# Performance work log

Hardware: AMD Instinct MI355X
Metric: run time of the kernel (lower is better)

## Reference

```python
import jax, jax.numpy as jnp
import numpy as np

B, C, H, W = 16, 256, 32, 32
NUM_LAYERS = 30
OUT = 16  # sqrt(out_channels)
EPS = 1e-5


def setup_inputs() -> dict:
    key = jax.random.key(0)
    k1, k2, k3 = jax.random.split(key, 3)
    x = jax.random.normal(k1, (B, C, H, W), dtype=jnp.float32)
    # delta_t ~ small positive values (module inits ~N(0.01, 0.005))
    delta_t = jax.random.uniform(k2, (NUM_LAYERS, 1), dtype=jnp.float32) * 0.02
    matrices = jax.random.normal(k3, (NUM_LAYERS, 1, 1, OUT, OUT), dtype=jnp.float32) * 0.1
    gamma = jnp.ones((H * W,), dtype=jnp.float32)   # BatchNorm2d weight, oc = i*i = H*W
    beta = jnp.zeros((H * W,), dtype=jnp.float32)   # BatchNorm2d bias
    return {"x": x, "delta_t": delta_t, "matrices": matrices, "gamma": gamma, "beta": beta}


def _bn_relu6(z, gamma, beta):
    # training-mode BatchNorm2d over channel axis 1 (channels = H*W), then ReLU6
    mean = jnp.mean(z, axis=(0, 2, 3), keepdims=True)
    var = jnp.mean(jnp.square(z - mean), axis=(0, 2, 3), keepdims=True)  # biased var
    zhat = (z - mean) * jax.lax.rsqrt(var + EPS)
    g = gamma.reshape(1, -1, 1, 1)
    b = beta.reshape(1, -1, 1, 1)
    return jnp.clip(zhat * g + b, 0.0, 6.0)


def reference(x, delta_t, matrices, gamma, beta):
    b, c, h, w = x.shape
    hw = h * w
    # feature_reshape: [B,C,H,W] -> [B,HW,C] -> [B,HW,out,out] (inn == out branch)
    x1 = x.reshape(b, c, hw).transpose(0, 2, 1).reshape(b, hw, OUT, OUT)
    dt = jnp.clip(delta_t, 0.0, 6.0)[:, 0]  # relu6(delta_t), shape [L]

    def step(y0, params):
        m, dtl = params  # m: [1,1,out,out] broadcasts elementwise against x1
        dydt = -y0 + _bn_relu6(y0 + m * x1, gamma, beta)
        return y0 + dtl * dydt, None

    y0, _ = jax.lax.scan(step, x1, (matrices, dt))
    # (y0 + x1): [B, HW, out, out] -> view [B,H,W,out*out] -> permute to [B,out*out,H,W]
    y = (y0 + x1).reshape(b, h, w, OUT * OUT).transpose(0, 3, 1, 2)
    return y
```

## Files before the change

### kernel.cpp

```cpp
#include <hip/hip_runtime.h>

typedef float v2f __attribute__((ext_vector_type(2)));
typedef float v4f __attribute__((ext_vector_type(4)));

#define HW      1024
#define NLAYERS 30
#define TPB     512

template <int CTRL, int RMASK>
__device__ __forceinline__ float dpp_add(float x) {
    int t = __builtin_amdgcn_update_dpp(0, __builtin_bit_cast(int, x),
                                        CTRL, RMASK, 0xf, true);
    return x + __builtin_bit_cast(float, t);
}
__device__ __forceinline__ float wave_sum64(float x) {
    x = dpp_add<0x111, 0xf>(x);
    x = dpp_add<0x112, 0xf>(x);
    x = dpp_add<0x114, 0xf>(x);
    x = dpp_add<0x118, 0xf>(x);
    x = dpp_add<0x142, 0xa>(x);
    x = dpp_add<0x143, 0xc>(x);
    return x;
}

__global__ __launch_bounds__(TPB, 4) void ode2ch(
    const float* __restrict__ x, const float* __restrict__ delta_t,
    const float* __restrict__ matrices, const float* __restrict__ gamma,
    const float* __restrict__ beta, float* __restrict__ out) {

    const int bid = blockIdx.x;
    const int gs  = ((bid & 7) << 6) | (bid >> 3);
    const int p0  = gs << 1;
    const int t   = threadIdx.x;
    const int c   = t & 255;
    const int bb0 = t >> 8;
    const int wid = t >> 6;
    const int lane = t & 63;

    __shared__ v4f red[2][8];

    v2f x1[8], y[8], z[8];
#pragma unroll
    for (int i = 0; i < 8; ++i) {
        const size_t off = (size_t)((2 * i + bb0) * 256 + c) * HW + p0;
        x1[i] = *(const v2f*)(x + off);
        y[i]  = x1[i];
    }

    const v2f gp2 = *(const v2f*)(gamma + p0);
    const v2f bp2 = *(const v2f*)(beta + p0);

    {
        const float m0 = matrices[c];
        const v2f M0 = {m0, m0};
        v2f s = {0.f, 0.f}, q = {0.f, 0.f};
#pragma unroll
        for (int i = 0; i < 8; ++i) {
            z[i] = __builtin_elementwise_fma(M0, x1[i], y[i]);
            s += z[i];
            q = __builtin_elementwise_fma(z[i], z[i], q);
        }
        const float sx = wave_sum64(s.x), sy = wave_sum64(s.y);
        const float qx = wave_sum64(q.x), qy = wave_sum64(q.y);
        if (lane == 63) { v4f w; w.x = sx; w.y = sy; w.z = qx; w.w = qy; red[0][wid] = w; }
    }

    float m_cur  = matrices[256 + c];
    float dt_cur = delta_t[0];
    float dt_nxt = delta_t[1];
    __syncthreads();

    for (int k = 0; k < NLAYERS - 1; ++k) {
        const int k2 = (k + 2 < NLAYERS) ? k + 2 : NLAYERS - 1;
        const float m_nxt  = matrices[k2 * 256 + c];
        const float dt_nn  = delta_t[k2];

        const v4f* r = red[k & 1];
        v4f a0 = r[0] + r[1], a1 = r[2] + r[3], a2 = r[4] + r[5], a3 = r[6] + r[7];
        const v4f acc = (a0 + a1) + (a2 + a3);

        const float dtk = __builtin_amdgcn_fmed3f(dt_cur, 0.0f, 6.0f);
        const v2f mean2 = {acc.x * (1.0f / 4096.0f), acc.y * (1.0f / 4096.0f)};
        const v2f msq2  = {acc.z * (1.0f / 4096.0f), acc.w * (1.0f / 4096.0f)};
        const v2f var2  = __builtin_elementwise_fma(-mean2, mean2, msq2);
        v2f rstd; rstd.x = rsqrtf(var2.x + 1e-5f); rstd.y = rsqrtf(var2.y + 1e-5f);
        const v2f g2 = gp2 * rstd;
        const v2f b2 = __builtin_elementwise_fma(-mean2, g2, bp2);
        const v2f dt2 = {dtk, dtk};
        const v2f M2  = {m_cur, m_cur};

        v2f s = {0.f, 0.f}, q = {0.f, 0.f};
#pragma unroll
        for (int i = 0; i < 8; ++i) {
            v2f a = __builtin_elementwise_fma(z[i], g2, b2);
            a.x = __builtin_amdgcn_fmed3f(a.x, 0.0f, 6.0f);
            a.y = __builtin_amdgcn_fmed3f(a.y, 0.0f, 6.0f);
            const v2f d = a - y[i];
            y[i] = __builtin_elementwise_fma(dt2, d, y[i]);
            z[i] = __builtin_elementwise_fma(M2, x1[i], y[i]);
            s += z[i];
            q = __builtin_elementwise_fma(z[i], z[i], q);
        }
        const float sx = wave_sum64(s.x), sy = wave_sum64(s.y);
        const float qx = wave_sum64(q.x), qy = wave_sum64(q.y);
        if (lane == 63) { v4f w; w.x = sx; w.y = sy; w.z = qx; w.w = qy; red[(k + 1) & 1][wid] = w; }

        m_cur = m_nxt; dt_cur = dt_nxt; dt_nxt = dt_nn;
        __syncthreads();
    }

    {
        const v4f* r = red[(NLAYERS - 1) & 1];
        v4f a0 = r[0] + r[1], a1 = r[2] + r[3], a2 = r[4] + r[5], a3 = r[6] + r[7];
        const v4f acc = (a0 + a1) + (a2 + a3);

        const float dtk = __builtin_amdgcn_fmed3f(dt_cur, 0.0f, 6.0f);
        const v2f mean2 = {acc.x * (1.0f / 4096.0f), acc.y * (1.0f / 4096.0f)};
        const v2f msq2  = {acc.z * (1.0f / 4096.0f), acc.w * (1.0f / 4096.0f)};
        const v2f var2  = __builtin_elementwise_fma(-mean2, mean2, msq2);
        v2f rstd; rstd.x = rsqrtf(var2.x + 1e-5f); rstd.y = rsqrtf(var2.y + 1e-5f);
        const v2f g2 = gp2 * rstd;
        const v2f b2 = __builtin_elementwise_fma(-mean2, g2, bp2);
        const v2f dt2 = {dtk, dtk};

#pragma unroll
        for (int i = 0; i < 8; ++i) {
            v2f a = __builtin_elementwise_fma(z[i], g2, b2);
            a.x = __builtin_amdgcn_fmed3f(a.x, 0.0f, 6.0f);
            a.y = __builtin_amdgcn_fmed3f(a.y, 0.0f, 6.0f);
            const v2f d = a - y[i];
            const v2f yf = __builtin_elementwise_fma(dt2, d, y[i]);
            const size_t off = (size_t)((2 * i + bb0) * 256 + c) * HW + p0;
            *(v2f*)(out + off) = yf + x1[i];
        }
    }
}

extern "C" void kernel_launch(void* const* d_in, const int* in_sizes, int n_in,
                              void* d_out, int out_size, void* d_ws, size_t ws_size,
                              hipStream_t stream) {
    const float* x        = (const float*)d_in[0];
    const float* delta_t  = (const float*)d_in[1];
    const float* matrices = (const float*)d_in[2];
    const float* gamma    = (const float*)d_in[3];
    const float* beta     = (const float*)d_in[4];
    float* out = (float*)d_out;

    ode2ch<<<dim3(HW / 2), dim3(TPB), 0, stream>>>(x, delta_t, matrices, gamma, beta, out);
}
```

Baseline: 123.0 us.

## Halve block size and split two BN channels into separately pipelined passes

Each block now uses 256 threads, and each thread holds 16 batch-channel elements per pixel instead of 8. Data is transposed in registers so each pixel channel (A/B) is a packed pair across two batch rows. The per-layer work runs as two separate channel passes, each with its own wave reduction, so the reduction of one channel can overlap the arithmetic of the other. The update is rewritten as y*(1-dt)+dt*a using inline v_pk_fma, and the loop is unrolled by two. The cost is higher register pressure and half as many threads per block, which lowers occupancy.

```diff
diff --git a/kernel.cpp b/kernel.cpp
--- a/kernel.cpp
+++ b/kernel.cpp
@@ -5,7 +5,20 @@
 
 #define HW      1024
 #define NLAYERS 30
-#define TPB     512
+#define TPB     256
+
+static __device__ __forceinline__ v2f pk_fma(v2f a, v2f b, v2f c) {
+    v2f d; asm("v_pk_fma_f32 %0, %1, %2, %3" : "=v"(d) : "v"(a), "v"(b), "v"(c));
+    return d;
+}
+static __device__ __forceinline__ v2f pk_add(v2f a, v2f b) {
+    v2f d; asm("v_pk_add_f32 %0, %1, %2" : "=v"(d) : "v"(a), "v"(b));
+    return d;
+}
+static __device__ __forceinline__ v2f pk_mul(v2f a, v2f b) {
+    v2f d; asm("v_pk_mul_f32 %0, %1, %2" : "=v"(d) : "v"(a), "v"(b));
+    return d;
+}
 
 template <int CTRL, int RMASK>
 __device__ __forceinline__ float dpp_add(float x) {
@@ -23,7 +36,41 @@
     return x;
 }
 
-__global__ __launch_bounds__(TPB, 4) void ode2ch(
+struct Stats { v2f g2, b2; };
+
+__device__ __forceinline__ Stats bn_stats(const v4f* r, float gp, float bp) {
+    const v4f r0 = r[0], r1 = r[1];
+    const float S = (r0.x + r0.z) + (r1.x + r1.z);
+    const float Q = (r0.y + r0.w) + (r1.y + r1.w);
+    const float mean = S * (1.0f / 4096.0f);
+    const float var  = fmaf(-mean, mean, Q * (1.0f / 4096.0f));
+    const float rstd = rsqrtf(var + 1e-5f);
+    const float g    = gp * rstd;
+    const float b    = fmaf(-mean, g, bp);
+    Stats st; st.g2 = (v2f){g, g}; st.b2 = (v2f){b, b};
+    return st;
+}
+
+__device__ __forceinline__ void pass_channel(const v2f (&x1)[8], v2f (&y)[8], v2f (&z)[8],
+                                             v2f g2, v2f b2, v2f dt2, v2f om2, v2f M2,
+                                             float& s_out, float& q_out) {
+    v2f s = {0.f, 0.f}, q = {0.f, 0.f};
+#pragma unroll
+    for (int i = 0; i < 8; ++i) {
+        v2f a = pk_fma(z[i], g2, b2);
+        a.x = __builtin_amdgcn_fmed3f(a.x, 0.0f, 6.0f);
+        a.y = __builtin_amdgcn_fmed3f(a.y, 0.0f, 6.0f);
+        y[i] = pk_mul(om2, y[i]);
+        y[i] = pk_fma(dt2, a, y[i]);
+        z[i] = pk_fma(M2, x1[i], y[i]);
+        s = pk_add(s, z[i]);
+        q = pk_fma(z[i], z[i], q);
+    }
+    s_out = wave_sum64(s.x + s.y);
+    q_out = wave_sum64(q.x + q.y);
+}
+
+__global__ __launch_bounds__(TPB, 2) void ode_pipe(
     const float* __restrict__ x, const float* __restrict__ delta_t,
     const float* __restrict__ matrices, const float* __restrict__ gamma,
     const float* __restrict__ beta, float* __restrict__ out) {
@@ -32,106 +79,107 @@
     const int gs  = ((bid & 7) << 6) | (bid >> 3);
     const int p0  = gs << 1;
     const int t   = threadIdx.x;
-    const int c   = t & 255;
-    const int bb0 = t >> 8;
     const int wid = t >> 6;
     const int lane = t & 63;
 
-    __shared__ v4f red[2][8];
+    __shared__ __align__(16) v2f red[2][2][4];
 
-    v2f x1[8], y[8], z[8];
+    v2f xA[8], xB[8], yA[8], yB[8], zA[8], zB[8];
 #pragma unroll
-    for (int i = 0; i < 8; ++i) {
-        const size_t off = (size_t)((2 * i + bb0) * 256 + c) * HW + p0;
-        x1[i] = *(const v2f*)(x + off);
-        y[i]  = x1[i];
+    for (int k = 0; k < 8; ++k) {
+        const size_t e0 = (size_t)(t + 512 * k);
+        const size_t e1 = e0 + 256;
+        const v2f u = *(const v2f*)(x + e0 * HW + p0);
+        const v2f v = *(const v2f*)(x + e1 * HW + p0);
+        xA[k] = (v2f){u.x, v.x};
+        xB[k] = (v2f){u.y, v.y};
+        yA[k] = xA[k];
+        yB[k] = xB[k];
     }
 
-    const v2f gp2 = *(const v2f*)(gamma + p0);
-    const v2f bp2 = *(const v2f*)(beta + p0);
+    const v2f gp = *(const v2f*)(gamma + p0);
+    const v2f bp = *(const v2f*)(beta + p0);
 
     {
-        const float m0 = matrices[c];
+        const float m0 = matrices[t];
         const v2f M0 = {m0, m0};
-        v2f s = {0.f, 0.f}, q = {0.f, 0.f};
+        v2f sA = {0.f, 0.f}, qA = {0.f, 0.f}, sB = {0.f, 0.f}, qB = {0.f, 0.f};
 #pragma unroll
         for (int i = 0; i < 8; ++i) {
-            z[i] = __builtin_elementwise_fma(M0, x1[i], y[i]);
-            s += z[i];
-            q = __builtin_elementwise_fma(z[i], z[i], q);
+            zA[i] = pk_fma(M0, xA[i], yA[i]);
+            sA = pk_add(sA, zA[i]);
+            qA = pk_fma(zA[i], zA[i], qA);
+            zB[i] = pk_fma(M0, xB[i], yB[i]);
+            sB = pk_add(sB, zB[i]);
+            qB = pk_fma(zB[i], zB[i], qB);
         }
-        const float sx = wave_sum64(s.x), sy = wave_sum64(s.y);
-        const float qx = wave_sum64(q.x), qy = wave_sum64(q.y);
-        if (lane == 63) { v4f w; w.x = sx; w.y = sy; w.z = qx; w.w = qy; red[0][wid] = w; }
+        const float sa = wave_sum64(sA.x + sA.y), qa = wave_sum64(qA.x + qA.y);
+        const float sb = wave_sum64(sB.x + sB.y), qb = wave_sum64(qB.x + qB.y);
+        if (lane == 63) {
+            red[0][0][wid] = (v2f){sa, qa};
+            red[0][1][wid] = (v2f){sb, qb};
+        }
     }
 
-    float m_cur  = matrices[256 + c];
+    float m_cur  = matrices[256 + t];
     float dt_cur = delta_t[0];
     float dt_nxt = delta_t[1];
     __syncthreads();
 
+#pragma unroll 2
     for (int k = 0; k < NLAYERS - 1; ++k) {
         const int k2 = (k + 2 < NLAYERS) ? k + 2 : NLAYERS - 1;
-        const float m_nxt  = matrices[k2 * 256 + c];
-        const float dt_nn  = delta_t[k2];
+        const float m_nxt = matrices[k2 * 256 + t];
+        const float dt_nn = delta_t[k2];
 
-        const v4f* r = red[k & 1];
-        v4f a0 = r[0] + r[1], a1 = r[2] + r[3], a2 = r[4] + r[5], a3 = r[6] + r[7];
-        const v4f acc = (a0 + a1) + (a2 + a3);
+        const int par = k & 1;
+        const Stats stA = bn_stats((const v4f*)&red[par][0][0], gp.x, bp.x);
+        const Stats stB = bn_stats((const v4f*)&red[par][1][0], gp.y, bp.y);
 
         const float dtk = __builtin_amdgcn_fmed3f(dt_cur, 0.0f, 6.0f);
-        const v2f mean2 = {acc.x * (1.0f / 4096.0f), acc.y * (1.0f / 4096.0f)};
-        const v2f msq2  = {acc.z * (1.0f / 4096.0f), acc.w * (1.0f / 4096.0f)};
-        const v2f var2  = __builtin_elementwise_fma(-mean2, mean2, msq2);
-        v2f rstd; rstd.x = rsqrtf(var2.x + 1e-5f); rstd.y = rsqrtf(var2.y + 1e-5f);
-        const v2f g2 = gp2 * rstd;
-        const v2f b2 = __builtin_elementwise_fma(-mean2, g2, bp2);
         const v2f dt2 = {dtk, dtk};
+        const v2f om2 = {1.0f - dtk, 1.0f - dtk};
         const v2f M2  = {m_cur, m_cur};
 
-        v2f s = {0.f, 0.f}, q = {0.f, 0.f};
-#pragma unroll
-        for (int i = 0; i < 8; ++i) {
-            v2f a = __builtin_elementwise_fma(z[i], g2, b2);
-            a.x = __builtin_amdgcn_fmed3f(a.x, 0.0f, 6.0f);
-            a.y = __builtin_amdgcn_fmed3f(a.y, 0.0f, 6.0f);
-            const v2f d = a - y[i];
-            y[i] = __builtin_elementwise_fma(dt2, d, y[i]);
-            z[i] = __builtin_elementwise_fma(M2, x1[i], y[i]);
-            s += z[i];
-            q = __builtin_elementwise_fma(z[i], z[i], q);
-        }
-        const float sx = wave_sum64(s.x), sy = wave_sum64(s.y);
-        const float qx = wave_sum64(q.x), qy = wave_sum64(q.y);
-        if (lane == 63) { v4f w; w.x = sx; w.y = sy; w.z = qx; w.w = qy; red[(k + 1) & 1][wid] = w; }
+        float sa, qa, sb, qb;
+        pass_channel(xA, yA, zA, stA.g2, stA.b2, dt2, om2, M2, sa, qa);
+        if (lane == 63) red[par ^ 1][0][wid] = (v2f){sa, qa};
+        pass_channel(xB, yB, zB, stB.g2, stB.b2, dt2, om2, M2, sb, qb);
+        if (lane == 63) red[par ^ 1][1][wid] = (v2f){sb, qb};
 
         m_cur = m_nxt; dt_cur = dt_nxt; dt_nxt = dt_nn;
         __syncthreads();
     }
 
     {
-        const v4f* r = red[(NLAYERS - 1) & 1];
-        v4f a0 = r[0] + r[1], a1 = r[2] + r[3], a2 = r[4] + r[5], a3 = r[6] + r[7];
-        const v4f acc = (a0 + a1) + (a2 + a3);
-
+        const Stats stA = bn_stats((const v4f*)&red[1][0][0], gp.x, bp.x);
+        const Stats stB = bn_stats((const v4f*)&red[1][1][0], gp.y, bp.y);
         const float dtk = __builtin_amdgcn_fmed3f(dt_cur, 0.0f, 6.0f);
-        const v2f mean2 = {acc.x * (1.0f / 4096.0f), acc.y * (1.0f / 4096.0f)};
-        const v2f msq2  = {acc.z * (1.0f / 4096.0f), acc.w * (1.0f / 4096.0f)};
-        const v2f var2  = __builtin_elementwise_fma(-mean2, mean2, msq2);
-        v2f rstd; rstd.x = rsqrtf(var2.x + 1e-5f); rstd.y = rsqrtf(var2.y + 1e-5f);
-        const v2f g2 = gp2 * rstd;
-        const v2f b2 = __builtin_elementwise_fma(-mean2, g2, bp2);
         const v2f dt2 = {dtk, dtk};
+        const v2f om2 = {1.0f - dtk, 1.0f - dtk};
 
 #pragma unroll
         for (int i = 0; i < 8; ++i) {
-            v2f a = __builtin_elementwise_fma(z[i], g2, b2);
-            a.x = __builtin_amdgcn_fmed3f(a.x, 0.0f, 6.0f);
-            a.y = __builtin_amdgcn_fmed3f(a.y, 0.0f, 6.0f);
-            const v2f d = a - y[i];
-            const v2f yf = __builtin_elementwise_fma(dt2, d, y[i]);
-            const size_t off = (size_t)((2 * i + bb0) * 256 + c) * HW + p0;
-            *(v2f*)(out + off) = yf + x1[i];
+            v2f aA = pk_fma(zA[i], stA.g2, stA.b2);
+            aA.x = __builtin_amdgcn_fmed3f(aA.x, 0.0f, 6.0f);
+            aA.y = __builtin_amdgcn_fmed3f(aA.y, 0.0f, 6.0f);
+            yA[i] = pk_mul(om2, yA[i]);
+            yA[i] = pk_fma(dt2, aA, yA[i]);
+            v2f aB = pk_fma(zB[i], stB.g2, stB.b2);
+            aB.x = __builtin_amdgcn_fmed3f(aB.x, 0.0f, 6.0f);
+            aB.y = __builtin_amdgcn_fmed3f(aB.y, 0.0f, 6.0f);
+            yB[i] = pk_mul(om2, yB[i]);
+            yB[i] = pk_fma(dt2, aB, yB[i]);
+        }
+
+#pragma unroll
+        for (int k = 0; k < 8; ++k) {
+            const size_t e0 = (size_t)(t + 512 * k);
+            const size_t e1 = e0 + 256;
+            const v2f u = {yA[k].x + xA[k].x, yB[k].x + xB[k].x};
+            const v2f v = {yA[k].y + xA[k].y, yB[k].y + xB[k].y};
+            *(v2f*)(out + e0 * HW + p0) = u;
+            *(v2f*)(out + e1 * HW + p0) = v;
         }
     }
 }
@@ -146,5 +194,5 @@
     const float* beta     = (const float*)d_in[4];
     float* out = (float*)d_out;
 
-    ode2ch<<<dim3(HW / 2), dim3(TPB), 0, stream>>>(x, delta_t, matrices, gamma, beta, out);
+    ode_pipe<<<dim3(HW / 2), dim3(TPB), 0, stream>>>(x, delta_t, matrices, gamma, beta, out);
 }
```

Result: faster. 117.7 us (-4.3%).
